# Kernel tuning notes

Hardware: AMD Instinct MI355X
Metric: run time of the kernel (lower is better)

The kernel has to match this reference:

```python
import jax, jax.numpy as jnp
import numpy as np

NUM_JOINTS = 21
K_ORDER = 2
IN_DIM, HID_DIM, OUT_DIM = 256, 128, 3
BATCH = 16384

# Standard 21-joint hand skeleton edges (wrist=0, 4 joints per finger)
HAND_EDGES = [[0,1],[1,2],[2,3],[3,4],
              [0,5],[5,6],[6,7],[7,8],
              [0,9],[9,10],[10,11],[11,12],
              [0,13],[13,14],[14,15],[15,16],
              [0,17],[17,18],[18,19],[19,20]]

def _adj_mx_from_edges(num_pts, edges):
    # symmetric 0/1 adjacency + self loops, then row-normalized (D^-1 (A+I))
    A = np.zeros((num_pts, num_pts), dtype=np.float32)
    for i, j in edges:
        A[i, j] = 1.0
        A[j, i] = 1.0
    A = A + np.eye(num_pts, dtype=np.float32)
    A = A / A.sum(axis=1, keepdims=True)
    return A

def _cheb_basis(adj, K):
    # normalized graph Laplacian: L = I - D^{-1/2} A D^{-1/2}
    N = adj.shape[0]
    d = jnp.power(jnp.sum(adj, axis=-1), -0.5)
    L = jnp.eye(N, dtype=adj.dtype) - (d[:, None] * adj) * d[None, :]
    # Chebyshev recursion: T0 = I, T1 = L, Tk = 2 L T_{k-1} - T_{k-2}
    Ts = [jnp.eye(N, dtype=adj.dtype), L]
    for _ in range(2, K):
        Ts.append(2.0 * (L @ Ts[-1]) - Ts[-2])
    return jnp.stack(Ts[:K], axis=0)  # [K, N, N]

_ADJ = jnp.asarray(_adj_mx_from_edges(NUM_JOINTS, HAND_EDGES))
_CHEB_T = _cheb_basis(_ADJ, K_ORDER)  # constant [K, 21, 21]

def _cheb_conv(x, W, b):
    # x: [B, N, C], W: [K, C, D], b: [1, 1, D]
    # result_k = T_k @ x @ W_k, summed over k
    return jnp.einsum('knm,bmc,kcd->bnd', _CHEB_T, x, W) + b

def setup_inputs() -> dict:
    key = jax.random.key(0)
    ks = jax.random.split(key, 7)
    s1 = 1.0 / np.sqrt(IN_DIM * K_ORDER)
    s2 = 1.0 / np.sqrt(HID_DIM * K_ORDER)
    return {
        'x':  jax.random.normal(ks[0], (BATCH, NUM_JOINTS, IN_DIM), dtype=jnp.float32),
        'W1': jax.random.normal(ks[1], (K_ORDER, IN_DIM, HID_DIM), dtype=jnp.float32) * s1,
        'b1': jax.random.normal(ks[2], (1, 1, HID_DIM), dtype=jnp.float32) * 0.01,
        'W2': jax.random.normal(ks[3], (K_ORDER, HID_DIM, HID_DIM), dtype=jnp.float32) * s2,
        'b2': jax.random.normal(ks[4], (1, 1, HID_DIM), dtype=jnp.float32) * 0.01,
        'W3': jax.random.normal(ks[5], (K_ORDER, HID_DIM, OUT_DIM), dtype=jnp.float32) * s2,
        'b3': jax.random.normal(ks[6], (1, 1, OUT_DIM), dtype=jnp.float32) * 0.01,
    }

def reference(x, W1, b1, W2, b2, W3, b3):
    h = jax.nn.leaky_relu(_cheb_conv(x, W1, b1), negative_slope=0.01)
    h = jax.nn.leaky_relu(_cheb_conv(h, W2, b2), negative_slope=0.01)
    return _cheb_conv(h, W3, b3)  # [B, 21, 3]
```

## Files before the change

kernel.cpp:

```cpp
#include <hip/hip_runtime.h>
#include <stdint.h>

typedef __bf16 bf16x8 __attribute__((ext_vector_type(8)));
typedef float  f32x4  __attribute__((ext_vector_type(4)));
typedef uint16_t u16x4 __attribute__((ext_vector_type(4)));

#define N_JOINT 21
#define TB 4
#define BATCH 16384
#define TILES 16
#define NBLK (BATCH / (TB * TILES))
#define NTHREAD 512

__device__ __forceinline__ uint32_t swz(uint32_t byteoff, uint32_t row) {
  return byteoff ^ ((row & 7u) << 4);
}
__device__ __forceinline__ uint16_t f2b(float v) {
  __bf16 b = (__bf16)v;
  return __builtin_bit_cast(uint16_t, b);
}

__device__ __forceinline__ uint32_t zto(int col, int row) {
  return (uint32_t)(col * 64 + ((((row >> 3) + col) & 7) << 3) + (row & 7));
}

__global__ void prep_weights(const float* __restrict__ W1, const float* __restrict__ W2,
                             const float* __restrict__ W3, uint16_t* __restrict__ ws) {
  uint16_t* wf1  = ws;
  uint16_t* wf2  = ws + 65536;
  uint16_t* wf3  = ws + 65536 + 32768;
  uint16_t* lhat = ws + 65536 + 32768 + 2048;
  for (int i = blockIdx.x * blockDim.x + threadIdx.x; i < 103424;
       i += gridDim.x * blockDim.x) {
    if (i < 65536) {
      int n = i >> 8, k = i & 255;
      float v = (n < 128) ? W1[k * 128 + n] : W1[32768 + k * 128 + (n - 128)];
      wf1[i] = f2b(v);
    } else if (i < 98304) {
      int j = i - 65536; int n = j >> 7, k = j & 127;
      float v = (n < 128) ? W2[k * 128 + n] : W2[16384 + k * 128 + (n - 128)];
      wf2[j] = f2b(v);
    } else if (i < 100352) {
      int j = i - 98304; int n = j >> 7, k = j & 127;
      float v = 0.f;
      if (n < 3)      v = W3[k * 3 + n];
      else if (n < 6) v = W3[384 + k * 3 + (n - 3)];
      wf3[j] = f2b(v);
    } else {
      int j = i - 100352; int m = j >> 6, k = j & 63;
      float v = 0.f;
      if (m < 42 && k < 42 && (m / 21 == k / 21)) {
        int n = m % 21, nk = k % 21;
        float invd = (n == 0) ? (1.f / 6.f) : ((((n - 1) & 3) == 3) ? 0.5f : (1.f / 3.f));
        if (nk == n) v = 1.f - invd;
        else {
          int pn = (n > 0) ? ((((n - 1) & 3) == 0) ? 0 : n - 1) : -1;
          int pk = (nk > 0) ? ((((nk - 1) & 3) == 0) ? 0 : nk - 1) : -1;
          if (pn == nk || pk == n) v = -invd;
        }
      }
      lhat[j] = f2b(v);
    }
  }
}

#define MFMA(d, va, vb) d = __builtin_amdgcn_mfma_f32_16x16x32_bf16(va, vb, d, 0, 0, 0)

#define ZSTORE(base, mt, v, c) { \
  u16x4 p_; p_[0] = f2b(v[0]); p_[1] = f2b(v[1]); p_[2] = f2b(v[2]); p_[3] = f2b(v[3]); \
  *(u16x4*)((base) + 2u * zto((c), mt * 16 + lk * 4)) = p_; \
}
#define HWR(dst, rb, mt, uv, bias) { \
  _Pragma("unroll") for (int rg_ = 0; rg_ < 4; ++rg_) { \
    int lr_ = mt * 16 + lk * 4 + rg_; \
    if (mt < 2 || lr_ < 42) { \
      int r_ = (rb) + lr_; \
      float h_ = uv[rg_] + bias; h_ = (h_ > 0.f) ? h_ : 0.01f * h_; \
      *(uint16_t*)(dst + swz(r_ * 256 + cu * 2, r_)) = f2b(h_); \
    } \
  } \
}
#define LHRD(fa, fb, mt) { \
  const int r_ = mt * 16 + l15; \
  fa = *(const bf16x8*)(lhsc + ((uint32_t)(r_ * 128 + lk * 16)      ^ ((r_ & 7u) << 4))); \
  fb = *(const bf16x8*)(lhsc + ((uint32_t)(r_ * 128 + 64 + lk * 16) ^ ((r_ & 7u) << 4))); \
}

__global__ __launch_bounds__(NTHREAD)
void cheb3_main(const float* __restrict__ xp,
                const uint16_t* __restrict__ wf1, const uint16_t* __restrict__ wf2,
                const uint16_t* __restrict__ wf3, const uint16_t* __restrict__ lhp,
                const float* __restrict__ b1p, const float* __restrict__ b2p,
                const float* __restrict__ b3p, float* __restrict__ outp)
{
  __shared__ __align__(16) uint16_t sA[96 * 256];
  __shared__ __align__(16) uint16_t sH[96 * 128];
  __shared__ __align__(16) uint16_t sH2[96 * 128];
  __shared__ __align__(16) uint16_t zt[2 * 128 * 64];
  __shared__ __align__(16) uint16_t zt3[2 * 16 * 64];
  __shared__ __align__(16) uint16_t lhs[48 * 64];

  const int tid  = threadIdx.x;
  const int wid  = tid >> 6;
  const int w8   = wid;
  const int lane = tid & 63;
  const int l15  = lane & 15;
  const int lk   = lane >> 4;
  char* sAc  = (char*)sA;
  char* sHc  = (char*)sH;
  char* sH2c = (char*)sH2;
  char* lhsc = (char*)lhs;
  char* ztH0 = (char*)zt;
  char* ztH1 = (char*)zt + 16384;
  char* zt3c = (char*)zt3;

  const int cu = w8 * 16 + l15;
  const float bias1 = b1p[cu];
  const float bias2 = b2p[cu];
  const float bias3 = (l15 < 3) ? b3p[l15] : 0.f;

  {
    uint4 z16 = make_uint4(0, 0, 0, 0);
    for (int i = tid; i < (2 * 128 * 64) / 8; i += NTHREAD)
      *(uint4*)((char*)zt + i * 16) = z16;
    if (tid < (2 * 16 * 64) / 8)
      *(uint4*)((char*)zt3 + tid * 16) = z16;
    if (tid < 384) {
      int f0 = tid * 8, ri = f0 >> 8, c = f0 & 255;
      int r = 42 + ri + ((ri >= 6) ? 42 : 0);
      *(uint4*)(sAc + swz(r * 512 + c * 2, r)) = z16;
    }
    if (tid < 192) {
      int f0 = tid * 8, ri = f0 >> 7, c = f0 & 127;
      int r = 42 + ri + ((ri >= 6) ? 42 : 0);
      *(uint4*)(sHc + swz(r * 256 + c * 2, r)) = z16;
      *(uint4*)(sH2c + swz(r * 256 + c * 2, r)) = z16;
    }
    if (tid < 384) {
      int row = tid >> 3, c = tid & 7;
      uint4 v = *(const uint4*)(lhp + row * 64 + c * 8);
      *(uint4*)(lhsc + ((uint32_t)(row * 128 + c * 16) ^ ((row & 7u) << 4))) = v;
    }
  }

  {
    const float* xg = xp + (size_t)(blockIdx.x * TILES) * (84 * 256);
    #pragma unroll
    for (int j = 0; j < 6; ++j) {
      int i = tid + j * NTHREAD;
      if (i < 2688) {
        int r84 = i >> 5, c8 = (i & 31) * 8;
        int sr = r84 + ((r84 >= 42) ? 6 : 0);
        float4 v0 = *(const float4*)(xg + r84 * 256 + c8);
        float4 v1 = *(const float4*)(xg + r84 * 256 + c8 + 4);
        bf16x8 o;
        o[0] = (__bf16)v0.x; o[1] = (__bf16)v0.y; o[2] = (__bf16)v0.z; o[3] = (__bf16)v0.w;
        o[4] = (__bf16)v1.x; o[5] = (__bf16)v1.y; o[6] = (__bf16)v1.z; o[7] = (__bf16)v1.w;
        *(bf16x8*)(sAc + swz(sr * 512 + c8 * 2, sr)) = o;
      }
    }
  }
  __syncthreads();

  const f32x4 zero4 = {0.f, 0.f, 0.f, 0.f};

  for (int t = 0; t < TILES; ++t) {
    const int gtile = blockIdx.x * TILES + t;
    const bool pf = (t + 1 < TILES);
    const float* xn = xp + (size_t)(gtile + 1) * (84 * 256);

    f32x4 u0 = zero4, u1 = zero4, u2 = zero4, u3 = zero4, u4 = zero4, u5 = zero4;
    f32x4 z0 = zero4, z1 = zero4, z2 = zero4, z3 = zero4, z4 = zero4, z5 = zero4;
    #pragma unroll 2
    for (int ch = 0; ch < 8; ++ch) {
      const bf16x8 wa_ = *(const bf16x8*)(wf1 + cu * 256 + ch * 32 + lk * 8);
      const bf16x8 wb_ = *(const bf16x8*)(wf1 + (cu + 128) * 256 + ch * 32 + lk * 8);
      const int kb_ = ch * 64 + lk * 16;
      {
        const int r0_ = 0 + l15, r1_ = 16 + l15, r2_ = 32 + l15;
        bf16x8 a0_ = *(const bf16x8*)(sAc + swz(r0_ * 512 + kb_, r0_));
        bf16x8 a1_ = *(const bf16x8*)(sAc + swz(r1_ * 512 + kb_, r1_));
        bf16x8 a2_ = *(const bf16x8*)(sAc + swz(r2_ * 512 + kb_, r2_));
        MFMA(u0, a0_, wa_); MFMA(u1, a1_, wa_); MFMA(u2, a2_, wa_);
        MFMA(z0, a0_, wb_); MFMA(z1, a1_, wb_); MFMA(z2, a2_, wb_);
      }
      {
        const int r3_ = 48 + l15, r4_ = 64 + l15, r5_ = 80 + l15;
        bf16x8 a3_ = *(const bf16x8*)(sAc + swz(r3_ * 512 + kb_, r3_));
        bf16x8 a4_ = *(const bf16x8*)(sAc + swz(r4_ * 512 + kb_, r4_));
        bf16x8 a5_ = *(const bf16x8*)(sAc + swz(r5_ * 512 + kb_, r5_));
        MFMA(u3, a3_, wa_); MFMA(u4, a4_, wa_); MFMA(u5, a5_, wa_);
        MFMA(z3, a3_, wb_); MFMA(z4, a4_, wb_); MFMA(z5, a5_, wb_);
      }
    }

    ZSTORE(ztH0, 0, z0, cu); ZSTORE(ztH0, 1, z1, cu); ZSTORE(ztH0, 2, z2, cu);
    ZSTORE(ztH1, 0, z3, cu); ZSTORE(ztH1, 1, z4, cu); ZSTORE(ztH1, 2, z5, cu);
    {
      bf16x8 fa, fb;
      bf16x8 bz0 = *(const bf16x8*)(ztH0 + 2u * zto(cu, 0 + lk * 8));
      bf16x8 bz1 = *(const bf16x8*)(ztH0 + 2u * zto(cu, 32 + lk * 8));
      LHRD(fa, fb, 0); MFMA(u0, fa, bz0); MFMA(u0, fb, bz1);
      LHRD(fa, fb, 1); MFMA(u1, fa, bz0); MFMA(u1, fb, bz1);
      LHRD(fa, fb, 2); MFMA(u2, fa, bz0); MFMA(u2, fb, bz1);
      bf16x8 bz2 = *(const bf16x8*)(ztH1 + 2u * zto(cu, 0 + lk * 8));
      bf16x8 bz3 = *(const bf16x8*)(ztH1 + 2u * zto(cu, 32 + lk * 8));
      LHRD(fa, fb, 0); MFMA(u3, fa, bz2); MFMA(u3, fb, bz3);
      LHRD(fa, fb, 1); MFMA(u4, fa, bz2); MFMA(u4, fb, bz3);
      LHRD(fa, fb, 2); MFMA(u5, fa, bz2); MFMA(u5, fb, bz3);
    }
    HWR(sHc, 0, 0, u0, bias1); HWR(sHc, 0, 1, u1, bias1); HWR(sHc, 0, 2, u2, bias1);
    HWR(sHc, 48, 0, u3, bias1); HWR(sHc, 48, 1, u4, bias1); HWR(sHc, 48, 2, u5, bias1);
    __syncthreads();

    if (pf) {
      #pragma unroll
      for (int j = 0; j < 6; ++j) {
        int i = tid + j * NTHREAD;
        if (i < 2688) {
          int r84 = i >> 5, c8 = (i & 31) * 8;
          int sr = r84 + ((r84 >= 42) ? 6 : 0);
          float4 v0 = *(const float4*)(xn + r84 * 256 + c8);
          float4 v1 = *(const float4*)(xn + r84 * 256 + c8 + 4);
          bf16x8 o;
          o[0] = (__bf16)v0.x; o[1] = (__bf16)v0.y; o[2] = (__bf16)v0.z; o[3] = (__bf16)v0.w;
          o[4] = (__bf16)v1.x; o[5] = (__bf16)v1.y; o[6] = (__bf16)v1.z; o[7] = (__bf16)v1.w;
          *(bf16x8*)(sAc + swz(sr * 512 + c8 * 2, sr)) = o;
        }
      }
    }

    u0 = zero4; u1 = zero4; u2 = zero4; u3 = zero4; u4 = zero4; u5 = zero4;
    z0 = zero4; z1 = zero4; z2 = zero4; z3 = zero4; z4 = zero4; z5 = zero4;
    #pragma unroll 2
    for (int ch = 0; ch < 4; ++ch) {
      const bf16x8 wa_ = *(const bf16x8*)(wf2 + cu * 128 + ch * 32 + lk * 8);
      const bf16x8 wb_ = *(const bf16x8*)(wf2 + (cu + 128) * 128 + ch * 32 + lk * 8);
      const int kb_ = ch * 64 + lk * 16;
      {
        const int r0_ = 0 + l15, r1_ = 16 + l15, r2_ = 32 + l15;
        bf16x8 a0_ = *(const bf16x8*)(sHc + swz(r0_ * 256 + kb_, r0_));
        bf16x8 a1_ = *(const bf16x8*)(sHc + swz(r1_ * 256 + kb_, r1_));
        bf16x8 a2_ = *(const bf16x8*)(sHc + swz(r2_ * 256 + kb_, r2_));
        MFMA(u0, a0_, wa_); MFMA(u1, a1_, wa_); MFMA(u2, a2_, wa_);
        MFMA(z0, a0_, wb_); MFMA(z1, a1_, wb_); MFMA(z2, a2_, wb_);
      }
      {
        const int r3_ = 48 + l15, r4_ = 64 + l15, r5_ = 80 + l15;
        bf16x8 a3_ = *(const bf16x8*)(sHc + swz(r3_ * 256 + kb_, r3_));
        bf16x8 a4_ = *(const bf16x8*)(sHc + swz(r4_ * 256 + kb_, r4_));
        bf16x8 a5_ = *(const bf16x8*)(sHc + swz(r5_ * 256 + kb_, r5_));
        MFMA(u3, a3_, wa_); MFMA(u4, a4_, wa_); MFMA(u5, a5_, wa_);
        MFMA(z3, a3_, wb_); MFMA(z4, a4_, wb_); MFMA(z5, a5_, wb_);
      }
    }

    ZSTORE(ztH0, 0, z0, cu); ZSTORE(ztH0, 1, z1, cu); ZSTORE(ztH0, 2, z2, cu);
    ZSTORE(ztH1, 0, z3, cu); ZSTORE(ztH1, 1, z4, cu); ZSTORE(ztH1, 2, z5, cu);
    {
      bf16x8 fa, fb;
      bf16x8 bz0 = *(const bf16x8*)(ztH0 + 2u * zto(cu, 0 + lk * 8));
      bf16x8 bz1 = *(const bf16x8*)(ztH0 + 2u * zto(cu, 32 + lk * 8));
      LHRD(fa, fb, 0); MFMA(u0, fa, bz0); MFMA(u0, fb, bz1);
      LHRD(fa, fb, 1); MFMA(u1, fa, bz0); MFMA(u1, fb, bz1);
      LHRD(fa, fb, 2); MFMA(u2, fa, bz0); MFMA(u2, fb, bz1);
      bf16x8 bz2 = *(const bf16x8*)(ztH1 + 2u * zto(cu, 0 + lk * 8));
      bf16x8 bz3 = *(const bf16x8*)(ztH1 + 2u * zto(cu, 32 + lk * 8));
      LHRD(fa, fb, 0); MFMA(u3, fa, bz2); MFMA(u3, fb, bz3);
      LHRD(fa, fb, 1); MFMA(u4, fa, bz2); MFMA(u4, fb, bz3);
      LHRD(fa, fb, 2); MFMA(u5, fa, bz2); MFMA(u5, fb, bz3);
    }
    HWR(sH2c, 0, 0, u0, bias2); HWR(sH2c, 0, 1, u1, bias2); HWR(sH2c, 0, 2, u2, bias2);
    HWR(sH2c, 48, 0, u3, bias2); HWR(sH2c, 48, 1, u4, bias2); HWR(sH2c, 48, 2, u5, bias2);
    __syncthreads();

    {
      const int duty = t & 7;
      if (w8 == duty || w8 == (duty ^ 1)) {
        const int h3 = (w8 == duty) ? 0 : 1;
        char* zt3H = zt3c + h3 * 2048;
        const int rb3 = h3 * 48;
        f32x4 c30 = zero4, c31 = zero4, c32 = zero4;
        #pragma unroll 2
        for (int ch = 0; ch < 4; ++ch) {
          const bf16x8 w3_ = *(const bf16x8*)(wf3 + l15 * 128 + ch * 32 + lk * 8);
          const int kb_ = ch * 64 + lk * 16;
          const int r0_ = rb3 + l15, r1_ = rb3 + 16 + l15, r2_ = rb3 + 32 + l15;
          bf16x8 a0_ = *(const bf16x8*)(sH2c + swz(r0_ * 256 + kb_, r0_));
          bf16x8 a1_ = *(const bf16x8*)(sH2c + swz(r1_ * 256 + kb_, r1_));
          bf16x8 a2_ = *(const bf16x8*)(sH2c + swz(r2_ * 256 + kb_, r2_));
          MFMA(c30, a0_, w3_); MFMA(c31, a1_, w3_); MFMA(c32, a2_, w3_);
        }
        if (l15 >= 3 && l15 < 6) {
          ZSTORE(zt3H, 0, c30, l15 - 3); ZSTORE(zt3H, 1, c31, l15 - 3); ZSTORE(zt3H, 2, c32, l15 - 3);
        }
        {
          bf16x8 fa, fb;
          bf16x8 b30 = *(const bf16x8*)(zt3H + 2u * zto(l15, 0 + lk * 8));
          bf16x8 b31 = *(const bf16x8*)(zt3H + 2u * zto(l15, 32 + lk * 8));
          LHRD(fa, fb, 0); MFMA(c30, fa, b30); MFMA(c30, fb, b31);
          LHRD(fa, fb, 1); MFMA(c31, fa, b30); MFMA(c31, fb, b31);
          LHRD(fa, fb, 2); MFMA(c32, fa, b30); MFMA(c32, fb, b31);
        }
        if (l15 < 3) {
          #define OUT3(mt, v) { \
            const int rb_ = mt * 16 + lk * 4; \
            _Pragma("unroll") \
            for (int rg = 0; rg < 4; ++rg) { \
              int r = rb_ + rg; \
              if (r < 42) { \
                int e = r / 21, n = r - e * 21; \
                outp[((size_t)(gtile * TB + h3 * 2 + e) * N_JOINT + n) * 3 + l15] = v[rg] + bias3; \
              } \
            } \
          }
          OUT3(0, c30); OUT3(1, c31); OUT3(2, c32);
          #undef OUT3
        }
      }
    }
  }
}

extern "C" void kernel_launch(void* const* d_in, const int* in_sizes, int n_in,
                              void* d_out, int out_size, void* d_ws, size_t ws_size,
                              hipStream_t stream) {
  const float* xp  = (const float*)d_in[0];
  const float* W1p = (const float*)d_in[1];
  const float* b1p = (const float*)d_in[2];
  const float* W2p = (const float*)d_in[3];
  const float* b2p = (const float*)d_in[4];
  const float* W3p = (const float*)d_in[5];
  const float* b3p = (const float*)d_in[6];
  uint16_t* ws = (uint16_t*)d_ws;

  hipLaunchKernelGGL(prep_weights, dim3(202), dim3(512), 0, stream, W1p, W2p, W3p, ws);

  const uint16_t* wf1 = ws;
  const uint16_t* wf2 = ws + 65536;
  const uint16_t* wf3 = ws + 65536 + 32768;
  const uint16_t* lhp = ws + 65536 + 32768 + 2048;
  hipLaunchKernelGGL(cheb3_main, dim3(NBLK), dim3(NTHREAD), 0, stream,
                     xp, wf1, wf2, wf3, lhp, b1p, b2p, b3p, (float*)d_out);
}
```

Measured before the change: 188.6 us.

## Software-pipeline next-tile x prefetch into registers across layer compute

Global loads for the next tile's input are now issued into registers before layer-1 compute and again before layer-2 compute. The bf16 conversion and shared-memory writes happen later, after the compute they were hidden behind. Before, each load was followed at once by its LDS write, which exposed global memory latency. The cost is 24 extra live VGPRs per thread, which may raise register pressure or cause spills at 512 threads.

```diff
diff --git a/kernel.cpp b/kernel.cpp
--- a/kernel.cpp
+++ b/kernel.cpp
@@ -86,6 +86,41 @@
   fb = *(const bf16x8*)(lhsc + ((uint32_t)(r_ * 128 + 64 + lk * 16) ^ ((r_ & 7u) << 4))); \
 }
 
+#define PF_ISSUE(p0, p1, j, src) { \
+  const int i_ = tid + j * NTHREAD; \
+  const int r_ = i_ >> 5, c8_ = (i_ & 31) * 8; \
+  p0 = *(const float4*)(src + r_ * 256 + c8_); \
+  p1 = *(const float4*)(src + r_ * 256 + c8_ + 4); \
+}
+#define PF_ISSUE_G(p0, p1, j, src) { \
+  const int i_ = tid + j * NTHREAD; \
+  if (i_ < 2688) { \
+    const int r_ = i_ >> 5, c8_ = (i_ & 31) * 8; \
+    p0 = *(const float4*)(src + r_ * 256 + c8_); \
+    p1 = *(const float4*)(src + r_ * 256 + c8_ + 4); \
+  } \
+}
+#define PF_WRITE(p0, p1, j) { \
+  const int i_ = tid + j * NTHREAD; \
+  const int r84_ = i_ >> 5, c8_ = (i_ & 31) * 8; \
+  const int sr_ = r84_ + ((r84_ >= 42) ? 6 : 0); \
+  bf16x8 o_; \
+  o_[0] = (__bf16)p0.x; o_[1] = (__bf16)p0.y; o_[2] = (__bf16)p0.z; o_[3] = (__bf16)p0.w; \
+  o_[4] = (__bf16)p1.x; o_[5] = (__bf16)p1.y; o_[6] = (__bf16)p1.z; o_[7] = (__bf16)p1.w; \
+  *(bf16x8*)(sAc + swz(sr_ * 512 + c8_ * 2, sr_)) = o_; \
+}
+#define PF_WRITE_G(p0, p1, j) { \
+  const int i_ = tid + j * NTHREAD; \
+  if (i_ < 2688) { \
+    const int r84_ = i_ >> 5, c8_ = (i_ & 31) * 8; \
+    const int sr_ = r84_ + ((r84_ >= 42) ? 6 : 0); \
+    bf16x8 o_; \
+    o_[0] = (__bf16)p0.x; o_[1] = (__bf16)p0.y; o_[2] = (__bf16)p0.z; o_[3] = (__bf16)p0.w; \
+    o_[4] = (__bf16)p1.x; o_[5] = (__bf16)p1.y; o_[6] = (__bf16)p1.z; o_[7] = (__bf16)p1.w; \
+    *(bf16x8*)(sAc + swz(sr_ * 512 + c8_ * 2, sr_)) = o_; \
+  } \
+}
+
 __global__ __launch_bounds__(NTHREAD)
 void cheb3_main(const float* __restrict__ xp,
                 const uint16_t* __restrict__ wf1, const uint16_t* __restrict__ wf2,
@@ -169,6 +204,9 @@
     const bool pf = (t + 1 < TILES);
     const float* xn = xp + (size_t)(gtile + 1) * (84 * 256);
 
+    float4 pA0, pA1, pA2, pA3, pA4, pA5;
+    if (pf) { PF_ISSUE(pA0, pA1, 0, xn); PF_ISSUE(pA2, pA3, 1, xn); PF_ISSUE(pA4, pA5, 2, xn); }
+
     f32x4 u0 = zero4, u1 = zero4, u2 = zero4, u3 = zero4, u4 = zero4, u5 = zero4;
     f32x4 z0 = zero4, z1 = zero4, z2 = zero4, z3 = zero4, z4 = zero4, z5 = zero4;
     #pragma unroll 2
@@ -214,20 +252,8 @@
     __syncthreads();
 
     if (pf) {
-      #pragma unroll
-      for (int j = 0; j < 6; ++j) {
-        int i = tid + j * NTHREAD;
-        if (i < 2688) {
-          int r84 = i >> 5, c8 = (i & 31) * 8;
-          int sr = r84 + ((r84 >= 42) ? 6 : 0);
-          float4 v0 = *(const float4*)(xn + r84 * 256 + c8);
-          float4 v1 = *(const float4*)(xn + r84 * 256 + c8 + 4);
-          bf16x8 o;
-          o[0] = (__bf16)v0.x; o[1] = (__bf16)v0.y; o[2] = (__bf16)v0.z; o[3] = (__bf16)v0.w;
-          o[4] = (__bf16)v1.x; o[5] = (__bf16)v1.y; o[6] = (__bf16)v1.z; o[7] = (__bf16)v1.w;
-          *(bf16x8*)(sAc + swz(sr * 512 + c8 * 2, sr)) = o;
-        }
-      }
+      PF_WRITE(pA0, pA1, 0); PF_WRITE(pA2, pA3, 1); PF_WRITE(pA4, pA5, 2);
+      PF_ISSUE(pA0, pA1, 3, xn); PF_ISSUE(pA2, pA3, 4, xn); PF_ISSUE_G(pA4, pA5, 5, xn);
     }
 
     u0 = zero4; u1 = zero4; u2 = zero4; u3 = zero4; u4 = zero4; u5 = zero4;
@@ -272,6 +298,8 @@
     }
     HWR(sH2c, 0, 0, u0, bias2); HWR(sH2c, 0, 1, u1, bias2); HWR(sH2c, 0, 2, u2, bias2);
     HWR(sH2c, 48, 0, u3, bias2); HWR(sH2c, 48, 1, u4, bias2); HWR(sH2c, 48, 2, u5, bias2);
+
+    if (pf) { PF_WRITE(pA0, pA1, 3); PF_WRITE(pA2, pA3, 4); PF_WRITE_G(pA4, pA5, 5); }
     __syncthreads();
 
     {
```

Result: faster. 182.0 us (-3.5%).
